# Kernel optimization log

Measured on AMD Instinct MI355X. Metric: run time of the kernel, lower is better.

## Reference

```python
import jax, jax.numpy as jnp
import numpy as np

EMBED = 1024
HEADS = 16
HEAD_DIM = EMBED // HEADS
MAX_REL = 16


def setup_inputs() -> dict:
    key = jax.random.key(0)
    ks = jax.random.split(key, 8)
    s = 0.02
    x = jax.random.normal(ks[0], (4, 2048, EMBED), dtype=jnp.float32)
    Wq = jax.random.normal(ks[1], (EMBED, EMBED), dtype=jnp.float32) * s
    bq = jnp.zeros((EMBED,), dtype=jnp.float32)
    Wk = jax.random.normal(ks[2], (EMBED, EMBED), dtype=jnp.float32) * s
    bk = jnp.zeros((EMBED,), dtype=jnp.float32)
    Wv = jax.random.normal(ks[3], (EMBED, EMBED), dtype=jnp.float32) * s
    bv = jnp.zeros((EMBED,), dtype=jnp.float32)
    rel_bias = jax.random.normal(ks[4], (2 * MAX_REL + 1, HEADS), dtype=jnp.float32) * s
    return {"x": x, "Wq": Wq, "bq": bq, "Wk": Wk, "bk": bk, "Wv": Wv, "bv": bv, "rel_bias": rel_bias}


def reference(x, Wq, bq, Wk, bk, Wv, bv, rel_bias):
    B, S, _ = x.shape
    # projections (Linear: x @ W + b, with W stored [in, out])
    q = (x @ Wq + bq).reshape(B, S, HEADS, HEAD_DIM).transpose(0, 2, 1, 3)  # [B,H,S,D]
    k = (x @ Wk + bk).reshape(B, S, HEADS, HEAD_DIM).transpose(0, 2, 1, 3)
    v = (x @ Wv + bv).reshape(B, S, HEADS, HEAD_DIM).transpose(0, 2, 1, 3)
    scores = jnp.einsum('bhqd,bhkd->bhqk', q, k) / jnp.sqrt(jnp.float32(HEAD_DIM))
    pos = jnp.arange(S)
    rel = jnp.clip(pos[None, :] - pos[:, None], -MAX_REL, MAX_REL) + MAX_REL  # [S,S]
    bias = rel_bias[rel]                      # [S,S,H]
    scores = scores + bias.transpose(2, 0, 1)[None]  # [B,H,S,S]
    probs = jax.nn.softmax(scores, axis=-1)
    # dropout is identity in eval mode
    out = jnp.einsum('bhqk,bhkd->bhqd', probs, v)
    return out.transpose(0, 2, 1, 3).reshape(B, S, EMBED)
```

## Files before the change

kernel.cpp:

```cpp
#include <hip/hip_runtime.h>

#define EMBED 1024
#define HEADS 16
#define HDIM  64
#define SEQ   2048
#define BATCH 4
#define MTOT  (BATCH*SEQ)

typedef __attribute__((ext_vector_type(8)))  short short8;
typedef __attribute__((ext_vector_type(4)))  float f32x4;
typedef __attribute__((ext_vector_type(16))) float f32x16;

#define GLOAD_LDS16(g, l) \
  __builtin_amdgcn_global_load_lds((const __attribute__((address_space(1))) void*)(g), \
                                   (__attribute__((address_space(3))) void*)(l), 16, 0, 0)

__device__ inline unsigned short f2bf(float f) {
  union { float f; unsigned u; } v; v.f = f;
  unsigned r = v.u + 0x7FFF + ((v.u >> 16) & 1);
  return (unsigned short)(r >> 16);
}

__device__ inline unsigned cvtpk(float lo, float hi) {
  unsigned r;
  asm("v_cvt_pk_bf16_f32 %0, %1, %2" : "=v"(r) : "v"(lo), "v"(hi));
  return r;
}

__device__ inline float vexp2(float x) {
  float r;
  asm("v_exp_f32 %0, %1" : "=v"(r) : "v"(x));
  return r;
}

#define PLSWAP(a, b) asm("v_permlane32_swap_b32 %0, %1" : "+v"(a), "+v"(b))

__device__ inline short8 mk8(unsigned w0, unsigned w1, unsigned w2, unsigned w3) {
  union { unsigned u[4]; short8 s; } x;
  x.u[0] = w0; x.u[1] = w1; x.u[2] = w2; x.u[3] = w3;
  return x.s;
}

__global__ void cvt_x(const float* __restrict__ x, unsigned short* __restrict__ xb) {
  int i = (blockIdx.x * blockDim.x + threadIdx.x) * 8;
  f32x4 a = *(const f32x4*)(x + i);
  f32x4 b = *(const f32x4*)(x + i + 4);
  unsigned short o[8];
  o[0]=f2bf(a[0]); o[1]=f2bf(a[1]); o[2]=f2bf(a[2]); o[3]=f2bf(a[3]);
  o[4]=f2bf(b[0]); o[5]=f2bf(b[1]); o[6]=f2bf(b[2]); o[7]=f2bf(b[3]);
  *(short8*)(xb + i) = *(short8*)o;
}

__global__ void transpose_w(const float* __restrict__ Wq, const float* __restrict__ Wk,
                            const float* __restrict__ Wv, unsigned short* __restrict__ Wtb) {
  __shared__ float tile[32][33];
  int wsel = blockIdx.z;
  const float* W = wsel == 0 ? Wq : (wsel == 1 ? Wk : Wv);
  int k0 = blockIdx.x * 32, n0 = blockIdx.y * 32;
  int tx = threadIdx.x & 31, ty = threadIdx.x >> 5;
  for (int i = 0; i < 4; ++i)
    tile[ty + i*8][tx] = W[(k0 + ty + i*8) * EMBED + n0 + tx];
  __syncthreads();
  unsigned short* o = Wtb + wsel * EMBED * EMBED;
  for (int i = 0; i < 4; ++i)
    o[(n0 + ty + i*8) * EMBED + k0 + tx] = f2bf(tile[tx][ty + i*8]);
}

__global__ __launch_bounds__(256)
void qkv_gemm(const unsigned short* __restrict__ xb, const unsigned short* __restrict__ Wtb,
              const float* __restrict__ bq, const float* __restrict__ bk, const float* __restrict__ bv,
              unsigned short* __restrict__ Qb, unsigned short* __restrict__ Kb,
              unsigned short* __restrict__ Vt) {
  __shared__ unsigned short As[128 * 72];
  __shared__ unsigned short Bs[128 * 72];
  int wsel = blockIdx.z;
  int m0 = blockIdx.x * 128, n0 = blockIdx.y * 128;
  int t = threadIdx.x, lane = t & 63, wave = t >> 6;
  int wr = wave >> 1, wc = wave & 1;
  int lr = lane & 15, lg = lane >> 4;
  const unsigned short* Wt = Wtb + wsel * (EMBED * EMBED);
  const float* bias = wsel == 0 ? bq : (wsel == 1 ? bk : bv);

  f32x4 acc[4][4] = {};

  for (int kt = 0; kt < EMBED / 64; ++kt) {
    int k0 = kt * 64;
    for (int i = 0; i < 4; ++i) {
      int c = i * 256 + t;
      int row = c >> 3, col8 = c & 7;
      short8 va = *(const short8*)(xb + (m0 + row) * EMBED + k0 + col8 * 8);
      short8 vb = *(const short8*)(Wt + (n0 + row) * EMBED + k0 + col8 * 8);
      *(short8*)(As + row * 72 + col8 * 8) = va;
      *(short8*)(Bs + row * 72 + col8 * 8) = vb;
    }
    __syncthreads();
    for (int kk = 0; kk < 2; ++kk) {
      short8 af[4], bfr[4];
      for (int mf = 0; mf < 4; ++mf)
        af[mf] = *(const short8*)(As + (wr * 64 + mf * 16 + lr) * 72 + kk * 32 + lg * 8);
      for (int nf = 0; nf < 4; ++nf)
        bfr[nf] = *(const short8*)(Bs + (wc * 64 + nf * 16 + lr) * 72 + kk * 32 + lg * 8);
      for (int mf = 0; mf < 4; ++mf)
        for (int nf = 0; nf < 4; ++nf)
          acc[mf][nf] = __builtin_amdgcn_mfma_f32_16x16x32_bf16(af[mf], bfr[nf], acc[mf][nf], 0, 0, 0);
    }
    __syncthreads();
  }

  const float SCLQ = 0.125f * 1.44269504088896340736f;
  for (int nf = 0; nf < 4; ++nf) {
    int n = n0 + wc * 64 + nf * 16 + lr;
    float bval = bias[n];
    int h = n >> 6, d = n & 63;
    for (int mf = 0; mf < 4; ++mf) {
      for (int r = 0; r < 4; ++r) {
        int m = m0 + wr * 64 + mf * 16 + lg * 4 + r;
        int b = m >> 11, s = m & 2047;
        float oval = acc[mf][nf][r] + bval;
        if (wsel == 0) oval *= SCLQ;
        unsigned short bfv = f2bf(oval);
        if (wsel == 0)      Qb[((b * HEADS + h) * SEQ + s) * HDIM + d] = bfv;
        else if (wsel == 1) Kb[((b * HEADS + h) * SEQ + s) * HDIM + d] = bfv;
        else                Vt[((b * HEADS + h) * HDIM + d) * SEQ + s] = bfv;
      }
    }
  }
}

__global__ __launch_bounds__(256)
void attn(const unsigned short* __restrict__ Qb, const unsigned short* __restrict__ Kb,
          const unsigned short* __restrict__ Vt, const float* __restrict__ rel_bias,
          float* __restrict__ out) {
  __shared__ unsigned short KVs[16384];
  __shared__ float bias_l[33];
  __shared__ float dld[4][32];
  int bh = blockIdx.y;
  int b = bh >> 4, h = bh & 15;
  int t = threadIdx.x, lane = t & 63, wave = t >> 6;
  int l31 = lane & 31, hi = lane >> 5;
  const float LOG2E = 1.44269504088896340736f;
  if (t < 33) bias_l[t] = rel_bias[t * HEADS + h] * LOG2E;

  int qw0 = blockIdx.x * 128 + wave * 32;
  const unsigned short* Qp = Qb + (bh * SEQ + qw0) * HDIM;
  const unsigned short* Kp = Kb + bh * SEQ * HDIM;
  const unsigned short* Vp = Vt + bh * HDIM * SEQ;

  short8 qf[4];
  #pragma unroll
  for (int ks = 0; ks < 4; ++ks)
    qf[ks] = *(const short8*)(Qp + l31 * HDIM + ks * 16 + hi * 8);

  unsigned rbo[2][4];
  #pragma unroll
  for (int rs = 0; rs < 2; ++rs)
    #pragma unroll
    for (int ks = 0; ks < 4; ++ks) {
      int row = rs * 32 + l31;
      rbo[rs][ks] = (unsigned)((row << 7) + ((((ks << 1) | hi) ^ (row & 7)) << 4));
    }
  #define LDK(rs, ks, BUF) \
    (*(const short8*)((const char*)KVs + rbo[rs][ks] + (BUF) * 8192))
  #define LDVv(rs, ks, BUF) \
    (*(const short8*)((const char*)KVs + rbo[rs][ks] + 16384 + (BUF) * 8192))

  f32x16 O0 = {}, O1 = {};
  float ls0 = 0.f, ls1 = 0.f;
  int q = qw0 + l31;

  int srow0 = (wave << 4) + (lane >> 3);
  int sslot = lane & 7;

  #define STAGE(BUF, key0_)                                                          \
    for (int j = 0; j < 2; ++j) {                                                    \
      int srow = srow0 + j * 8;                                                      \
      int cs = sslot ^ (srow & 7);                                                   \
      GLOAD_LDS16(Kp + ((key0_) + srow) * HDIM + cs * 8,                             \
                  &KVs[(BUF) * 4096 + (((wave << 4) + j * 8) << 6)]);                \
      GLOAD_LDS16(Vp + srow * SEQ + (key0_) + cs * 8,                                \
                  &KVs[8192 + (BUF) * 4096 + (((wave << 4) + j * 8) << 6)]);         \
    }

  STAGE(0, 0)
  __syncthreads();
  float cbLo = bias_l[0], cbHi = bias_l[32];

  #define PROC(SACC, KOFF, BUF)  {                                                   \
    float pv[16];                                                                    \
    int kbase = key0 + (KOFF);                                                       \
    if (kbase >= qw0 + 47) {                                                         \
      _Pragma("unroll") for (int r = 0; r < 16; ++r)                                 \
        pv[r] = vexp2(SACC[r] + cbHi);                                               \
    } else if (kbase <= qw0 - 47) {                                                  \
      _Pragma("unroll") for (int r = 0; r < 16; ++r)                                 \
        pv[r] = vexp2(SACC[r] + cbLo);                                               \
    } else {                                                                         \
      _Pragma("unroll") for (int r = 0; r < 16; ++r) {                               \
        int key = kbase + (r & 3) + 8 * (r >> 2) + 4 * hi;                           \
        int rel = key - q;                                                           \
        rel = rel < -16 ? -16 : (rel > 16 ? 16 : rel);                               \
        pv[r] = vexp2(SACC[r] + bias_l[rel + 16]);                                   \
      }                                                                              \
    }                                                                                \
    ls0 += ((pv[0] + pv[1]) + (pv[2] + pv[3])) + ((pv[4] + pv[5]) + (pv[6] + pv[7]));\
    ls1 += ((pv[8] + pv[9]) + (pv[10] + pv[11])) + ((pv[12] + pv[13]) + (pv[14] + pv[15]));\
                       \
    unsigned a0 = cvtpk(pv[0], pv[1]),  a1 = cvtpk(pv[4], pv[5]);   PLSWAP(a0, a1);  \
    unsigned a2 = cvtpk(pv[2], pv[3]),  a3 = cvtpk(pv[6], pv[7]);   PLSWAP(a2, a3);  \
    unsigned b0 = cvtpk(pv[8], pv[9]),  b1 = cvtpk(pv[12], pv[13]); PLSWAP(b0, b1);  \
    unsigned b2 = cvtpk(pv[10], pv[11]), b3 = cvtpk(pv[14], pv[15]); PLSWAP(b2, b3); \
    short8 pa0 = mk8(a0, a2, a1, a3);                                                \
    short8 pa1 = mk8(b0, b2, b1, b3);                                                \
    O0 = __builtin_amdgcn_mfma_f32_32x32x16_bf16(pa0, LDVv(0, (KOFF)/16, BUF),     O0, 0, 0, 0); \
    O1 = __builtin_amdgcn_mfma_f32_32x32x16_bf16(pa0, LDVv(1, (KOFF)/16, BUF),     O1, 0, 0, 0); \
    O0 = __builtin_amdgcn_mfma_f32_32x32x16_bf16(pa1, LDVv(0, (KOFF)/16 + 1, BUF), O0, 0, 0, 0); \
    O1 = __builtin_amdgcn_mfma_f32_32x32x16_bf16(pa1, LDVv(1, (KOFF)/16 + 1, BUF), O1, 0, 0, 0); \
  }

  #define HALF(RS, KOFF, BUF)  {                                                     \
    f32x16 s_ = {};                                                                  \
    _Pragma("unroll") for (int ks = 0; ks < 4; ++ks)                                 \
      s_ = __builtin_amdgcn_mfma_f32_32x32x16_bf16(LDK(RS, ks, BUF), qf[ks], s_, 0, 0, 0); \
    PROC(s_, KOFF, BUF)                                                              \
  }

  #define PHASE(BUF, KEY0, DO_STAGE)  {                                              \
    int key0 = (KEY0);                                                               \
    if (DO_STAGE) { STAGE(BUF ^ 1, key0 + 64) }                                      \
    HALF(0, 0, BUF)                                                                  \
    __builtin_amdgcn_sched_barrier(0);     \
    HALF(1, 32, BUF)                                                                 \
    __syncthreads();                                                                 \
  }

  for (int kbp = 0; kbp < 16; ++kbp) {
    PHASE(0, (kbp * 2) * 64, 1)
    PHASE(1, (kbp * 2 + 1) * 64, kbp < 15)
  }

  float lsum = ls0 + ls1;
  float denom = lsum + __shfl_xor(lsum, 32, 64);
  if (lane < 32) dld[wave][l31] = 1.0f / denom;
  float* op = out + (b * SEQ + qw0) * EMBED + h * HDIM;
  #pragma unroll
  for (int r = 0; r < 16; ++r) {
    int ql = (r & 3) + 8 * (r >> 2) + 4 * hi;
    float inv = dld[wave][ql];
    op[ql * EMBED + l31]      = O0[r] * inv;
    op[ql * EMBED + 32 + l31] = O1[r] * inv;
  }
  #undef STAGE
  #undef LDK
  #undef LDVv
  #undef PROC
  #undef HALF
  #undef PHASE
}

extern "C" void kernel_launch(void* const* d_in, const int* in_sizes, int n_in,
                              void* d_out, int out_size, void* d_ws, size_t ws_size,
                              hipStream_t stream) {
  const float* x        = (const float*)d_in[0];
  const float* Wq       = (const float*)d_in[1];
  const float* bq       = (const float*)d_in[2];
  const float* Wk       = (const float*)d_in[3];
  const float* bk       = (const float*)d_in[4];
  const float* Wv       = (const float*)d_in[5];
  const float* bv       = (const float*)d_in[6];
  const float* rel_bias = (const float*)d_in[7];
  float* out = (float*)d_out;

  char* ws = (char*)d_ws;
  unsigned short* xb  = (unsigned short*)(ws);
  unsigned short* Wtb = (unsigned short*)(ws + 16777216);
  unsigned short* Qb  = (unsigned short*)(ws + 23068672);
  unsigned short* Kb  = (unsigned short*)(ws + 39845888);
  unsigned short* Vt  = (unsigned short*)(ws + 56623104);

  cvt_x<<<MTOT * EMBED / (256 * 8), 256, 0, stream>>>(x, xb);
  transpose_w<<<dim3(32, 32, 3), 256, 0, stream>>>(Wq, Wk, Wv, Wtb);
  qkv_gemm<<<dim3(MTOT / 128, EMBED / 128, 3), 256, 0, stream>>>(xb, Wtb, bq, bk, bv, Qb, Kb, Vt);
  attn<<<dim3(SEQ / 128, BATCH * HEADS), 256, 0, stream>>>(Qb, Kb, Vt, rel_bias, out);
}
```

Measured before the change: 207.5 us.

## Triple-buffer K/V tiles in attention with vmcnt-based partial waits

Moves the attention kernel's K/V staging from double to triple buffering in LDS. Two tiles are prefetched ahead, and each iteration waits with s_waitcnt vmcnt(4) plus a raw barrier instead of a full __syncthreads drain. This lets global-to-LDS loads overlap more compute and cuts full memory stalls per tile. LDS use grows from 32KB to 48KB per block, which may lower occupancy.

Measured after the change: 203.3 us. 2.1% less time.

```diff
diff --git a/kernel.cpp b/kernel.cpp
--- a/kernel.cpp
+++ b/kernel.cpp
@@ -131,7 +131,7 @@
 void attn(const unsigned short* __restrict__ Qb, const unsigned short* __restrict__ Kb,
           const unsigned short* __restrict__ Vt, const float* __restrict__ rel_bias,
           float* __restrict__ out) {
-  __shared__ unsigned short KVs[16384];
+  __shared__ unsigned short KVs[24576];
   __shared__ float bias_l[33];
   __shared__ float dld[4][32];
   int bh = blockIdx.y;
@@ -162,7 +162,7 @@
   #define LDK(rs, ks, BUF) \
     (*(const short8*)((const char*)KVs + rbo[rs][ks] + (BUF) * 8192))
   #define LDVv(rs, ks, BUF) \
-    (*(const short8*)((const char*)KVs + rbo[rs][ks] + 16384 + (BUF) * 8192))
+    (*(const short8*)((const char*)KVs + rbo[rs][ks] + 24576 + (BUF) * 8192))
 
   f32x16 O0 = {}, O1 = {};
   float ls0 = 0.f, ls1 = 0.f;
@@ -176,14 +176,16 @@
       int srow = srow0 + j * 8;                                                      \
       int cs = sslot ^ (srow & 7);                                                   \
       GLOAD_LDS16(Kp + ((key0_) + srow) * HDIM + cs * 8,                             \
-                  &KVs[(BUF) * 4096 + (((wave << 4) + j * 8) << 6)]);                \
+                  (char*)KVs + (BUF) * 8192 + ((((wave << 4) + j * 8) << 6) << 1));  \
       GLOAD_LDS16(Vp + srow * SEQ + (key0_) + cs * 8,                                \
-                  &KVs[8192 + (BUF) * 4096 + (((wave << 4) + j * 8) << 6)]);         \
-    }
-
-  STAGE(0, 0)
-  __syncthreads();
-  float cbLo = bias_l[0], cbHi = bias_l[32];
+                  (char*)KVs + 24576 + (BUF) * 8192 + ((((wave << 4) + j * 8) << 6) << 1)); \
+    }
+
+  #define WAITV4 asm volatile("s_waitcnt vmcnt(4)" ::: "memory");
+  #define WAITV0 asm volatile("s_waitcnt vmcnt(0)" ::: "memory");
+  #define BAR    __builtin_amdgcn_s_barrier();
+
+  float cbLo, cbHi;
 
   #define PROC(SACC, KOFF, BUF)  {                                                   \
     float pv[16];                                                                    \
@@ -204,7 +206,6 @@
     }                                                                                \
     ls0 += ((pv[0] + pv[1]) + (pv[2] + pv[3])) + ((pv[4] + pv[5]) + (pv[6] + pv[7]));\
     ls1 += ((pv[8] + pv[9]) + (pv[10] + pv[11])) + ((pv[12] + pv[13]) + (pv[14] + pv[15]));\
-                       \
     unsigned a0 = cvtpk(pv[0], pv[1]),  a1 = cvtpk(pv[4], pv[5]);   PLSWAP(a0, a1);  \
     unsigned a2 = cvtpk(pv[2], pv[3]),  a3 = cvtpk(pv[6], pv[7]);   PLSWAP(a2, a3);  \
     unsigned b0 = cvtpk(pv[8], pv[9]),  b1 = cvtpk(pv[12], pv[13]); PLSWAP(b0, b1);  \
@@ -224,19 +225,27 @@
     PROC(s_, KOFF, BUF)                                                              \
   }
 
-  #define PHASE(BUF, KEY0, DO_STAGE)  {                                              \
+  #define COMPUTE(BUF, KEY0)  {                                                      \
     int key0 = (KEY0);                                                               \
-    if (DO_STAGE) { STAGE(BUF ^ 1, key0 + 64) }                                      \
     HALF(0, 0, BUF)                                                                  \
-    __builtin_amdgcn_sched_barrier(0);     \
     HALF(1, 32, BUF)                                                                 \
-    __syncthreads();                                                                 \
-  }
-
-  for (int kbp = 0; kbp < 16; ++kbp) {
-    PHASE(0, (kbp * 2) * 64, 1)
-    PHASE(1, (kbp * 2 + 1) * 64, kbp < 15)
-  }
+  }
+
+  STAGE(0, 0)
+  STAGE(1, 64)
+  WAITV4
+  __syncthreads();
+  cbLo = bias_l[0]; cbHi = bias_l[32];
+
+  for (int i = 0; i < 10; ++i) {
+    int t3 = i * 3;
+    STAGE(2, (t3 + 2) * 64)  COMPUTE(0, t3 * 64)        WAITV4 BAR
+    STAGE(0, (t3 + 3) * 64)  COMPUTE(1, (t3 + 1) * 64)  WAITV4 BAR
+    STAGE(1, (t3 + 4) * 64)  COMPUTE(2, (t3 + 2) * 64)  WAITV4 BAR
+  }
+  COMPUTE(0, 30 * 64)
+  WAITV0 BAR
+  COMPUTE(1, 31 * 64)
 
   float lsum = ls0 + ls1;
   float denom = lsum + __shfl_xor(lsum, 32, 64);
@@ -254,7 +263,7 @@
   #undef LDVv
   #undef PROC
   #undef HALF
-  #undef PHASE
+  #undef COMPUTE
 }
 
 extern "C" void kernel_launch(void* const* d_in, const int* in_sizes, int n_in,
```
